# Optimization experiments

Hardware: AMD Instinct MI355X
Metric: run time of the kernel (lower is better)

Reference implementation:

```python
import jax, jax.numpy as jnp
import numpy as np

N = 50000      # nodes
E = 800000     # edges
IN = 64        # in_dim
HID = 32       # num_hidden (per head)
H1, H2, H3 = 4, 4, 6   # heads
C = 64         # num_classes
SLOPE = 0.2    # leaky relu negative slope


def setup_inputs() -> dict:
    key = jax.random.key(0)
    ks = jax.random.split(key, 13)
    p = lambda k, s: jax.random.normal(k, s, jnp.float32) * 0.05
    return {
        "src": jax.random.randint(ks[0], (E,), 0, N),
        "dst": jax.random.randint(ks[1], (E,), 0, N),
        "embed": p(ks[2], (N, IN)),
        "W0": p(ks[3], (IN, H1 * HID)),
        "al0": p(ks[4], (H1, HID)), "ar0": p(ks[5], (H1, HID)),
        "W1": p(ks[6], (H1 * HID, H2 * HID)),
        "al1": p(ks[7], (H2, HID)), "ar1": p(ks[8], (H2, HID)),
        "W2": p(ks[9], (H2 * HID, H3 * C)),
        "al2": p(ks[10], (H3, C)), "ar2": p(ks[11], (H3, C)),
        "Wres": p(ks[12], (H2 * HID, H3 * C)),
    }


def gat_conv(h, W, al, ar, src, dst, H, D, res=None):
    """One DGL-style GATConv (no dropout, eval mode)."""
    n = h.shape[0]
    feat = (h @ W).reshape(n, H, D)                      # [N,H,D]
    el = jnp.sum(feat * al, axis=-1)                     # [N,H]
    er = jnp.sum(feat * ar, axis=-1)                     # [N,H]
    e = jax.nn.leaky_relu(el[src] + er[dst], SLOPE)      # [E,H]
    # edge softmax over incoming edges of each dst node
    m = jax.lax.stop_gradient(jax.ops.segment_max(e, dst, num_segments=n))
    ex = jnp.exp(e - m[dst])
    s = jax.ops.segment_sum(ex, dst, num_segments=n)
    alpha = ex / jnp.where(s == 0.0, 1.0, s)[dst]        # [E,H]
    rst = jax.ops.segment_sum(feat[src] * alpha[:, :, None], dst, num_segments=n)
    if res is not None:
        rst = rst + res
    return rst                                           # [N,H,D]


def reference(src, dst, embed, W0, al0, ar0, W1, al1, ar1, W2, al2, ar2, Wres):
    h = embed
    # layer 0: no residual, elu, flatten heads
    h = jax.nn.elu(gat_conv(h, W0, al0, ar0, src, dst, H1, HID)).reshape(N, H1 * HID)
    # layer 1: residual is identity (in_dim == H2*HID)
    res1 = h.reshape(N, H2, HID)
    h = jax.nn.elu(gat_conv(h, W1, al1, ar1, src, dst, H2, HID, res=res1)).reshape(N, H2 * HID)
    # output layer: linear residual (dims differ), no activation, mean over heads
    res2 = (h @ Wres).reshape(N, H3, C)
    out = gat_conv(h, W2, al2, ar2, src, dst, H3, C, res=res2)
    return out.mean(axis=1)                              # [N,C]
```

## Files before the change

### kernel.cpp

```cpp
#include <hip/hip_runtime.h>
#include <hip/hip_bf16.h>
#include <cstdint>

#define NNODES 50000
#define NEDGES 800000
constexpr float SLOPE = 0.2f;

__device__ __forceinline__ float leakyf(float x){ return x > 0.f ? x : SLOPE * x; }
__device__ __forceinline__ float eluf(float x){ return x > 0.f ? x : expm1f(x); }

__global__ void hist_kernel(const int* __restrict__ dst, int* __restrict__ deg, int e){
  int i = blockIdx.x * 256 + threadIdx.x;
  if (i < e) atomicAdd(&deg[dst[i]], 1);
}

__global__ __launch_bounds__(256) void scan1_kernel(const int* __restrict__ deg,
    int* __restrict__ pre, int* __restrict__ bsum, int n){
  __shared__ int s[256];
  int t = threadIdx.x;
  int i = blockIdx.x * 256 + t;
  int v = (i < n) ? deg[i] : 0;
  s[t] = v;
  __syncthreads();
  #pragma unroll
  for (int off = 1; off < 256; off <<= 1){
    int x = (t >= off) ? s[t - off] : 0;
    __syncthreads();
    s[t] += x;
    __syncthreads();
  }
  if (i < n) pre[i] = s[t] - v;
  if (t == 255) bsum[blockIdx.x] = s[255];
}

__global__ __launch_bounds__(256) void scan2_kernel(int* __restrict__ bsum, int nb){
  __shared__ int s[256];
  int t = threadIdx.x;
  int v = (t < nb) ? bsum[t] : 0;
  s[t] = v;
  __syncthreads();
  #pragma unroll
  for (int off = 1; off < 256; off <<= 1){
    int x = (t >= off) ? s[t - off] : 0;
    __syncthreads();
    s[t] += x;
    __syncthreads();
  }
  if (t < nb) bsum[t] = s[t] - v;
}

__global__ __launch_bounds__(256) void scan3_kernel(const int* __restrict__ pre,
    const int* __restrict__ bsum, int* __restrict__ row, int* __restrict__ cur,
    int n, int etot){
  int i = blockIdx.x * 256 + threadIdx.x;
  if (i < n){
    int r = pre[i] + bsum[i >> 8];
    row[i] = r; cur[i] = r;
  }
  if (i == n) row[n] = etot;
}

__global__ void scatter_kernel(const int* __restrict__ src, const int* __restrict__ dst,
    int* __restrict__ cur, int* __restrict__ ssrc, int* __restrict__ sdst, int e){
  int i = blockIdx.x * 256 + threadIdx.x;
  if (i < e){
    int d = dst[i];
    int pos = atomicAdd(&cur[d], 1);
    ssrc[pos] = src[i];
    sdst[pos] = d;
  }
}

template<int K, bool ACC>
__global__ __launch_bounds__(256) void gemm_kernel(const float* __restrict__ A,
    const float* __restrict__ B, float* __restrict__ C, int n_rows, int n_cols){
  __shared__ float As[64][68];
  __shared__ float Bs[64][64];
  int tx = threadIdx.x & 15, ty = threadIdx.x >> 4;
  int row0 = blockIdx.x * 64, col0 = blockIdx.y * 64;
  float acc[4][4] = {};
  for (int k0 = 0; k0 < K; k0 += 64){
    for (int v = threadIdx.x; v < 1024; v += 256){
      int r = v >> 4, c = (v & 15) << 2;
      float4 val = make_float4(0.f, 0.f, 0.f, 0.f);
      int gr = row0 + r;
      if (gr < n_rows) val = *reinterpret_cast<const float4*>(&A[(size_t)gr * K + k0 + c]);
      *reinterpret_cast<float4*>(&As[r][c]) = val;
    }
    for (int v = threadIdx.x; v < 1024; v += 256){
      int r = v >> 4, c = (v & 15) << 2;
      *reinterpret_cast<float4*>(&Bs[r][c]) =
        *reinterpret_cast<const float4*>(&B[(size_t)(k0 + r) * n_cols + col0 + c]);
    }
    __syncthreads();
    #pragma unroll 8
    for (int k = 0; k < 64; ++k){
      float a[4], b[4];
      #pragma unroll
      for (int i = 0; i < 4; ++i) a[i] = As[ty * 4 + i][k];
      #pragma unroll
      for (int j = 0; j < 4; ++j) b[j] = Bs[k][tx * 4 + j];
      #pragma unroll
      for (int i = 0; i < 4; ++i)
        #pragma unroll
        for (int j = 0; j < 4; ++j)
          acc[i][j] += a[i] * b[j];
    }
    __syncthreads();
  }
  #pragma unroll
  for (int i = 0; i < 4; ++i){
    int gr = row0 + ty * 4 + i;
    if (gr < n_rows){
      float* cp = &C[(size_t)gr * n_cols + col0 + tx * 4];
      float4 v = make_float4(acc[i][0], acc[i][1], acc[i][2], acc[i][3]);
      if constexpr (ACC){
        float4 o = *reinterpret_cast<const float4*>(cp);
        v.x += o.x; v.y += o.y; v.z += o.z; v.w += o.w;
      }
      *reinterpret_cast<float4*>(cp) = v;
    }
  }
}

__global__ void wvec_kernel(const float* __restrict__ W, const float* __restrict__ al,
    const float* __restrict__ ar, float* __restrict__ wl, float* __restrict__ wr,
    int K, int H, int D){
  int idx = blockIdx.x * 256 + threadIdx.x;
  if (idx >= H * K) return;
  int h = idx / K, k = idx - h * K;
  const float* wrow = W + (size_t)k * H * D + h * D;
  const float* a = al + h * D;
  const float* b = ar + h * D;
  float sl = 0.f, sr = 0.f;
  for (int d = 0; d < D; ++d){ float wv = wrow[d]; sl += wv * a[d]; sr += wv * b[d]; }
  wl[idx] = sl; wr[idx] = sr;
}

template<int H, int K>
__global__ __launch_bounds__(256) void elrn_kernel(const float* __restrict__ x,
    const float* __restrict__ wl, const float* __restrict__ wr,
    float* __restrict__ el, float* __restrict__ er){
  __shared__ float wls[H * K], wrs[H * K];
  for (int v = threadIdx.x; v < H * K; v += 256){ wls[v] = wl[v]; wrs[v] = wr[v]; }
  __syncthreads();
  int n = blockIdx.x * 256 + threadIdx.x;
  if (n >= NNODES) return;
  const float* xr = x + (size_t)n * K;
  float accl[H] = {}, accr[H] = {};
  for (int k = 0; k < K; k += 4){
    float4 xv = *reinterpret_cast<const float4*>(xr + k);
    #pragma unroll
    for (int h = 0; h < H; ++h){
      const float* a = &wls[h * K + k];
      const float* b = &wrs[h * K + k];
      accl[h] += xv.x * a[0] + xv.y * a[1] + xv.z * a[2] + xv.w * a[3];
      accr[h] += xv.x * b[0] + xv.y * b[1] + xv.z * b[2] + xv.w * b[3];
    }
  }
  #pragma unroll
  for (int h = 0; h < H; ++h){ el[n * H + h] = accl[h]; er[n * H + h] = accr[h]; }
}

__global__ __launch_bounds__(256) void elr1_kernel(const float* __restrict__ feat,
    const float* __restrict__ al, const float* __restrict__ ar,
    float* __restrict__ el, float* __restrict__ er){
  __shared__ float als[128], ars[128];
  if (threadIdx.x < 128){ als[threadIdx.x] = al[threadIdx.x]; ars[threadIdx.x] = ar[threadIdx.x]; }
  __syncthreads();
  int n = blockIdx.x * 256 + threadIdx.x;
  if (n >= NNODES) return;
  const float* f = feat + (size_t)n * 128;
  float el4[4], er4[4];
  #pragma unroll
  for (int h = 0; h < 4; ++h){
    float sl = 0.f, sr = 0.f;
    #pragma unroll
    for (int d = 0; d < 32; d += 4){
      float4 fv = *reinterpret_cast<const float4*>(f + h * 32 + d);
      const float* a = &als[h * 32 + d];
      const float* b = &ars[h * 32 + d];
      sl += fv.x * a[0] + fv.y * a[1] + fv.z * a[2] + fv.w * a[3];
      sr += fv.x * b[0] + fv.y * b[1] + fv.z * b[2] + fv.w * b[3];
    }
    el4[h] = sl; er4[h] = sr;
  }
  *reinterpret_cast<float4*>(&el[n * 4]) = make_float4(el4[0], el4[1], el4[2], el4[3]);
  *reinterpret_cast<float4*>(&er[n * 4]) = make_float4(er4[0], er4[1], er4[2], er4[3]);
}

template<int H>
__global__ void ex_kernel(const float* __restrict__ el, const float* __restrict__ er,
    const int* __restrict__ ssrc, const int* __restrict__ sdst, float* __restrict__ ex, int e){
  int i = blockIdx.x * 256 + threadIdx.x;
  if (i >= e) return;
  int s = ssrc[i], d = sdst[i];
  if constexpr (H == 4){
    float4 a = *reinterpret_cast<const float4*>(&el[s * 4]);
    float4 b = *reinterpret_cast<const float4*>(&er[d * 4]);
    float4 o;
    o.x = expf(leakyf(a.x + b.x));
    o.y = expf(leakyf(a.y + b.y));
    o.z = expf(leakyf(a.z + b.z));
    o.w = expf(leakyf(a.w + b.w));
    *reinterpret_cast<float4*>(&ex[(size_t)i * 4]) = o;
  } else {
    const float* ap = &el[s * 6];
    const float* bp = &er[d * 6];
    float2 a0 = *reinterpret_cast<const float2*>(ap);
    float2 a1 = *reinterpret_cast<const float2*>(ap + 2);
    float2 a2 = *reinterpret_cast<const float2*>(ap + 4);
    float2 b0 = *reinterpret_cast<const float2*>(bp);
    float2 b1 = *reinterpret_cast<const float2*>(bp + 2);
    float2 b2 = *reinterpret_cast<const float2*>(bp + 4);
    float2 o0, o1, o2;
    o0.x = expf(leakyf(a0.x + b0.x)); o0.y = expf(leakyf(a0.y + b0.y));
    o1.x = expf(leakyf(a1.x + b1.x)); o1.y = expf(leakyf(a1.y + b1.y));
    o2.x = expf(leakyf(a2.x + b2.x)); o2.y = expf(leakyf(a2.y + b2.y));
    float* op = &ex[(size_t)i * 6];
    *reinterpret_cast<float2*>(op)     = o0;
    *reinterpret_cast<float2*>(op + 2) = o1;
    *reinterpret_cast<float2*>(op + 4) = o2;
  }
}

__global__ __launch_bounds__(1024) void agg_l0_kernel(const float* __restrict__ embed,
    const float* __restrict__ W0, const float* __restrict__ ex,
    const int* __restrict__ row, const int* __restrict__ ssrc, float* __restrict__ h1){
  __shared__ float W0t[128 * 68];
  __shared__ float gd[16][256];
  int w = threadIdx.x >> 6, lane = threadIdx.x & 63;
  for (int v = threadIdx.x; v < 2048; v += 1024){
    float4 val = *reinterpret_cast<const float4*>(&W0[(size_t)v << 2]);
    int k = (v << 2) >> 7;
    int c = (v << 2) & 127;
    W0t[(c + 0) * 68 + k] = val.x;
    W0t[(c + 1) * 68 + k] = val.y;
    W0t[(c + 2) * 68 + k] = val.z;
    W0t[(c + 3) * 68 + k] = val.w;
  }
  int n = blockIdx.x * 16 + w;
  int beg = __builtin_amdgcn_readfirstlane(row[n]);
  int end = __builtin_amdgcn_readfirstlane(row[n + 1]);
  float g0 = 0.f, g1 = 0.f, g2 = 0.f, g3 = 0.f;
  float t0 = 0.f, t1 = 0.f, t2 = 0.f, t3 = 0.f;
  int i = beg;
  for (; i + 8 <= end; i += 8){
    float v[8]; float4 e[8];
    #pragma unroll
    for (int u = 0; u < 8; ++u){
      int s = ssrc[i + u];
      v[u] = embed[(size_t)s * 64 + lane];
      e[u] = *reinterpret_cast<const float4*>(&ex[(size_t)(i + u) * 4]);
    }
    #pragma unroll
    for (int u = 0; u < 8; ++u){
      g0 += e[u].x * v[u]; g1 += e[u].y * v[u];
      g2 += e[u].z * v[u]; g3 += e[u].w * v[u];
      t0 += e[u].x; t1 += e[u].y; t2 += e[u].z; t3 += e[u].w;
    }
  }
  for (; i + 4 <= end; i += 4){
    float v[4]; float4 e[4];
    #pragma unroll
    for (int u = 0; u < 4; ++u){
      int s = ssrc[i + u];
      v[u] = embed[(size_t)s * 64 + lane];
      e[u] = *reinterpret_cast<const float4*>(&ex[(size_t)(i + u) * 4]);
    }
    #pragma unroll
    for (int u = 0; u < 4; ++u){
      g0 += e[u].x * v[u]; g1 += e[u].y * v[u];
      g2 += e[u].z * v[u]; g3 += e[u].w * v[u];
      t0 += e[u].x; t1 += e[u].y; t2 += e[u].z; t3 += e[u].w;
    }
  }
  for (; i < end; ++i){
    int s = ssrc[i];
    float ev = embed[(size_t)s * 64 + lane];
    float4 e = *reinterpret_cast<const float4*>(&ex[(size_t)i * 4]);
    g0 += e.x * ev; g1 += e.y * ev; g2 += e.z * ev; g3 += e.w * ev;
    t0 += e.x; t1 += e.y; t2 += e.z; t3 += e.w;
  }
  float i0 = t0 > 0.f ? 1.f / t0 : 0.f, i1 = t1 > 0.f ? 1.f / t1 : 0.f;
  float i2 = t2 > 0.f ? 1.f / t2 : 0.f, i3 = t3 > 0.f ? 1.f / t3 : 0.f;
  gd[w][lane] = g0 * i0; gd[w][64 + lane] = g1 * i1;
  gd[w][128 + lane] = g2 * i2; gd[w][192 + lane] = g3 * i3;
  __syncthreads();
  int c = threadIdx.x & 127, q = threadIdx.x >> 7;
  int h = c >> 5;
  const float4* wrow = reinterpret_cast<const float4*>(&W0t[c * 68]);
  const float4* gA = reinterpret_cast<const float4*>(&gd[2 * q][h * 64]);
  const float4* gB = reinterpret_cast<const float4*>(&gd[2 * q + 1][h * 64]);
  float o0 = 0.f, o1 = 0.f;
  #pragma unroll
  for (int k4 = 0; k4 < 16; ++k4){
    float4 wv = wrow[k4];
    float4 a = gA[k4], b = gB[k4];
    o0 += a.x * wv.x + a.y * wv.y + a.z * wv.z + a.w * wv.w;
    o1 += b.x * wv.x + b.y * wv.y + b.z * wv.z + b.w * wv.w;
  }
  int nb = blockIdx.x * 16;
  h1[(size_t)(nb + 2 * q) * 128 + c]     = eluf(o0);
  h1[(size_t)(nb + 2 * q + 1) * 128 + c] = eluf(o1);
}

__global__ __launch_bounds__(256) void agg32_kernel(const float* __restrict__ feat,
    const float* __restrict__ ex, const int* __restrict__ row, const int* __restrict__ ssrc,
    const float* __restrict__ resid, float* __restrict__ hout){
  int n = blockIdx.x * 4 + (threadIdx.x >> 6);
  if (n >= NNODES) return;
  int lane = threadIdx.x & 63, half = lane >> 5;
  int beg = __builtin_amdgcn_readfirstlane(row[n]);
  int end = __builtin_amdgcn_readfirstlane(row[n + 1]);
  float acc0 = 0.f, acc1 = 0.f, tA = 0.f, tB = 0.f;
  int i = beg;
  for (; i + 8 <= end; i += 8){
    float a[8], b[8], eA[8], eB[8];
    #pragma unroll
    for (int u = 0; u < 8; ++u){
      int s = ssrc[i + u];
      const float* fr = feat + (size_t)s * 128;
      a[u] = fr[lane]; b[u] = fr[64 + lane];
      float4 e = *reinterpret_cast<const float4*>(&ex[(size_t)(i + u) * 4]);
      eA[u] = half ? e.y : e.x;
      eB[u] = half ? e.w : e.z;
    }
    #pragma unroll
    for (int u = 0; u < 8; ++u){
      acc0 += eA[u] * a[u]; acc1 += eB[u] * b[u];
      tA += eA[u]; tB += eB[u];
    }
  }
  for (; i + 4 <= end; i += 4){
    float a[4], b[4], eA[4], eB[4];
    #pragma unroll
    for (int u = 0; u < 4; ++u){
      int s = ssrc[i + u];
      const float* fr = feat + (size_t)s * 128;
      a[u] = fr[lane]; b[u] = fr[64 + lane];
      float4 e = *reinterpret_cast<const float4*>(&ex[(size_t)(i + u) * 4]);
      eA[u] = half ? e.y : e.x;
      eB[u] = half ? e.w : e.z;
    }
    #pragma unroll
    for (int u = 0; u < 4; ++u){
      acc0 += eA[u] * a[u]; acc1 += eB[u] * b[u];
      tA += eA[u]; tB += eB[u];
    }
  }
  for (; i < end; ++i){
    int s = ssrc[i];
    const float* fr = feat + (size_t)s * 128;
    float4 e = *reinterpret_cast<const float4*>(&ex[(size_t)i * 4]);
    float eA = half ? e.y : e.x;
    float eB = half ? e.w : e.z;
    acc0 += eA * fr[lane]; acc1 += eB * fr[64 + lane];
    tA += eA; tB += eB;
  }
  float invA = tA > 0.f ? 1.f / tA : 0.f;
  float invB = tB > 0.f ? 1.f / tB : 0.f;
  float v0 = acc0 * invA, v1 = acc1 * invB;
  size_t o0 = (size_t)n * 128 + lane;
  v0 += resid[o0]; v1 += resid[o0 + 64];
  hout[o0]      = eluf(v0);
  hout[o0 + 64] = eluf(v1);
}

__global__ __launch_bounds__(256) void agg_l2_kernel(const float* __restrict__ h2,
    const float* __restrict__ ex, const int* __restrict__ row, const int* __restrict__ ssrc,
    float* __restrict__ gs, int node_off, int node_cnt){
  int rel = blockIdx.x * 4 + (threadIdx.x >> 6);
  if (rel >= node_cnt) return;
  int n = node_off + rel;
  int lane = threadIdx.x & 63;
  int beg = __builtin_amdgcn_readfirstlane(row[n]);
  int end = __builtin_amdgcn_readfirstlane(row[n + 1]);
  float t[6] = {};
  float ga[6] = {}, gb[6] = {};
  int i = beg;
  for (; i + 8 <= end; i += 8){
    float v0[8], v1[8];
    float2 ea[8], eb[8], ec[8];
    #pragma unroll
    for (int u = 0; u < 8; ++u){
      int s = ssrc[i + u];
      const float* hr = h2 + (size_t)s * 128;
      v0[u] = hr[lane]; v1[u] = hr[64 + lane];
      const float* e = &ex[(size_t)(i + u) * 6];
      ea[u] = *reinterpret_cast<const float2*>(e);
      eb[u] = *reinterpret_cast<const float2*>(e + 2);
      ec[u] = *reinterpret_cast<const float2*>(e + 4);
    }
    #pragma unroll
    for (int u = 0; u < 8; ++u){
      ga[0] += ea[u].x * v0[u]; gb[0] += ea[u].x * v1[u]; t[0] += ea[u].x;
      ga[1] += ea[u].y * v0[u]; gb[1] += ea[u].y * v1[u]; t[1] += ea[u].y;
      ga[2] += eb[u].x * v0[u]; gb[2] += eb[u].x * v1[u]; t[2] += eb[u].x;
      ga[3] += eb[u].y * v0[u]; gb[3] += eb[u].y * v1[u]; t[3] += eb[u].y;
      ga[4] += ec[u].x * v0[u]; gb[4] += ec[u].x * v1[u]; t[4] += ec[u].x;
      ga[5] += ec[u].y * v0[u]; gb[5] += ec[u].y * v1[u]; t[5] += ec[u].y;
    }
  }
  for (; i + 4 <= end; i += 4){
    float v0[4], v1[4];
    float2 ea[4], eb[4], ec[4];
    #pragma unroll
    for (int u = 0; u < 4; ++u){
      int s = ssrc[i + u];
      const float* hr = h2 + (size_t)s * 128;
      v0[u] = hr[lane]; v1[u] = hr[64 + lane];
      const float* e = &ex[(size_t)(i + u) * 6];
      ea[u] = *reinterpret_cast<const float2*>(e);
      eb[u] = *reinterpret_cast<const float2*>(e + 2);
      ec[u] = *reinterpret_cast<const float2*>(e + 4);
    }
    #pragma unroll
    for (int u = 0; u < 4; ++u){
      ga[0] += ea[u].x * v0[u]; gb[0] += ea[u].x * v1[u]; t[0] += ea[u].x;
      ga[1] += ea[u].y * v0[u]; gb[1] += ea[u].y * v1[u]; t[1] += ea[u].y;
      ga[2] += eb[u].x * v0[u]; gb[2] += eb[u].x * v1[u]; t[2] += eb[u].x;
      ga[3] += eb[u].y * v0[u]; gb[3] += eb[u].y * v1[u]; t[3] += eb[u].y;
      ga[4] += ec[u].x * v0[u]; gb[4] += ec[u].x * v1[u]; t[4] += ec[u].x;
      ga[5] += ec[u].y * v0[u]; gb[5] += ec[u].y * v1[u]; t[5] += ec[u].y;
    }
  }
  for (; i < end; ++i){
    int s = ssrc[i];
    const float* hr = h2 + (size_t)s * 128;
    float v0 = hr[lane], v1 = hr[64 + lane];
    const float* e = &ex[(size_t)i * 6];
    float2 a = *reinterpret_cast<const float2*>(e);
    float2 b = *reinterpret_cast<const float2*>(e + 2);
    float2 c = *reinterpret_cast<const float2*>(e + 4);
    ga[0] += a.x * v0; gb[0] += a.x * v1; t[0] += a.x;
    ga[1] += a.y * v0; gb[1] += a.y * v1; t[1] += a.y;
    ga[2] += b.x * v0; gb[2] += b.x * v1; t[2] += b.x;
    ga[3] += b.y * v0; gb[3] += b.y * v1; t[3] += b.y;
    ga[4] += c.x * v0; gb[4] += c.x * v1; t[4] += c.x;
    ga[5] += c.y * v0; gb[5] += c.y * v1; t[5] += c.y;
  }
  float inv[6];
  #pragma unroll
  for (int h = 0; h < 6; ++h) inv[h] = t[h] > 0.f ? 1.f / (6.f * t[h]) : 0.f;
  float* gr = gs + (size_t)rel * 768;
  #pragma unroll
  for (int h = 0; h < 6; ++h){
    gr[h * 128 + lane]      = ga[h] * inv[h];
    gr[h * 128 + 64 + lane] = gb[h] * inv[h];
  }
}

__global__ void w2r_kernel(const float* __restrict__ W2, float* __restrict__ W2r){
  int i = blockIdx.x * 256 + threadIdx.x;
  if (i >= 768 * 64) return;
  int hk = i >> 6, c = i & 63;
  int h = hk >> 7, k = hk & 127;
  W2r[i] = W2[(size_t)k * 384 + h * 64 + c];
}

__global__ void wresmean_kernel(const float* __restrict__ Wres, float* __restrict__ wm){
  int i = blockIdx.x * 256 + threadIdx.x;
  if (i < 128 * 64){
    int k = i >> 6, c = i & 63;
    float s = 0.f;
    #pragma unroll
    for (int h = 0; h < 6; ++h) s += Wres[k * 384 + h * 64 + c];
    wm[i] = s * (1.f / 6.f);
  }
}

extern "C" void kernel_launch(void* const* d_in, const int* in_sizes, int n_in,
                              void* d_out, int out_size, void* d_ws, size_t ws_size,
                              hipStream_t stream){
  const int*   src   = (const int*)d_in[0];
  const int*   dst   = (const int*)d_in[1];
  const float* embed = (const float*)d_in[2];
  const float* W0    = (const float*)d_in[3];
  const float* al0   = (const float*)d_in[4];
  const float* ar0   = (const float*)d_in[5];
  const float* W1    = (const float*)d_in[6];
  const float* al1   = (const float*)d_in[7];
  const float* ar1   = (const float*)d_in[8];
  const float* W2    = (const float*)d_in[9];
  const float* al2   = (const float*)d_in[10];
  const float* ar2   = (const float*)d_in[11];
  const float* Wres  = (const float*)d_in[12];
  float* out = (float*)d_out;

  char* p = (char*)d_ws;
  auto alloc = [&](size_t bytes) -> char* {
    char* r = p; p += (bytes + 255) & ~size_t(255); return r;
  };
  float* big  = (float*)alloc((size_t)25000 * 768 * 4);
  float* h1   = (float*)alloc((size_t)NNODES * 128 * 4);
  float* h2   = (float*)alloc((size_t)NNODES * 128 * 4);
  float* el   = (float*)alloc((size_t)NNODES * 6 * 4);
  float* er   = (float*)alloc((size_t)NNODES * 6 * 4);
  float* ex   = (float*)alloc((size_t)NEDGES * 6 * 4);
  float* wm   = (float*)alloc(128 * 64 * 4);
  float* W2r  = (float*)alloc(768 * 64 * 4);
  float* wl0  = (float*)alloc(4 * 64 * 4);
  float* wr0  = (float*)alloc(4 * 64 * 4);
  float* wl2  = (float*)alloc(6 * 128 * 4);
  float* wr2  = (float*)alloc(6 * 128 * 4);
  int* row    = (int*)alloc((NNODES + 1) * 4);
  int* cur    = (int*)alloc(NNODES * 4);
  int* deg    = (int*)alloc(NNODES * 4);
  int* pre    = (int*)alloc(NNODES * 4);
  int* bsum   = (int*)alloc(256 * 4);
  int* ssrc   = (int*)alloc(NEDGES * 4);
  int* sdst   = (int*)alloc(NEDGES * 4);

  const int NB = (NNODES + 255) / 256;

  hipMemsetAsync(deg, 0, NNODES * 4, stream);
  hist_kernel<<<(NEDGES + 255) / 256, 256, 0, stream>>>(dst, deg, NEDGES);
  scan1_kernel<<<NB, 256, 0, stream>>>(deg, pre, bsum, NNODES);
  scan2_kernel<<<1, 256, 0, stream>>>(bsum, NB);
  scan3_kernel<<<NB + 1, 256, 0, stream>>>(pre, bsum, row, cur, NNODES, NEDGES);
  scatter_kernel<<<(NEDGES + 255) / 256, 256, 0, stream>>>(src, dst, cur, ssrc, sdst, NEDGES);

  wvec_kernel<<<1, 256, 0, stream>>>(W0, al0, ar0, wl0, wr0, 64, 4, 32);
  wvec_kernel<<<3, 256, 0, stream>>>(W2, al2, ar2, wl2, wr2, 128, 6, 64);
  w2r_kernel<<<192, 256, 0, stream>>>(W2, W2r);
  wresmean_kernel<<<32, 256, 0, stream>>>(Wres, wm);

  const int GX = (NNODES + 63) / 64;
  const int GE = (NEDGES + 255) / 256;
  const int GN = (NNODES + 3) / 4;
  const int GNn = (NNODES + 255) / 256;

  elrn_kernel<4, 64><<<GNn, 256, 0, stream>>>(embed, wl0, wr0, el, er);
  ex_kernel<4><<<GE, 256, 0, stream>>>(el, er, ssrc, sdst, ex, NEDGES);
  agg_l0_kernel<<<NNODES / 16, 1024, 0, stream>>>(embed, W0, ex, row, ssrc, h1);

  gemm_kernel<128, false><<<dim3(GX, 2), 256, 0, stream>>>(h1, W1, big, NNODES, 128);
  elr1_kernel<<<GNn, 256, 0, stream>>>(big, al1, ar1, el, er);
  ex_kernel<4><<<GE, 256, 0, stream>>>(el, er, ssrc, sdst, ex, NEDGES);
  agg32_kernel<<<GN, 256, 0, stream>>>(big, ex, row, ssrc, h1, h2);

  elrn_kernel<6, 128><<<GNn, 256, 0, stream>>>(h2, wl2, wr2, el, er);
  ex_kernel<6><<<GE, 256, 0, stream>>>(el, er, ssrc, sdst, ex, NEDGES);
  gemm_kernel<128, false><<<dim3(GX, 1), 256, 0, stream>>>(h2, wm, out, NNODES, 64);
  const int HALF = 25000;
  for (int half = 0; half < 2; ++half){
    int off = half * HALF;
    agg_l2_kernel<<<(HALF + 3) / 4, 256, 0, stream>>>(h2, ex, row, ssrc, big, off, HALF);
    gemm_kernel<768, true><<<dim3((HALF + 63) / 64, 1), 256, 0, stream>>>(
        big, W2r, out + (size_t)off * 64, HALF, 64);
  }
}
```

Measured before the change: 587.8 us.

## Fill sorted dst from CSR rows and restructure layer-0 aggregation

The scatter kernel no longer writes sdst at scattered positions. A new per-node kernel fills sdst contiguously from the CSR row offsets instead. In agg_l0, the softmax denominators are computed first with a lane-parallel pass and a wave shuffle reduction, which removes the per-edge t accumulations from the main loop, and the 4-edge unrolled tail loop is dropped. W0 is now kept in shared memory in its original layout, without the transpose, and the projection loop reads it as scalars. This adds an extra kernel launch and a second read of ex per node in exchange for cheaper scatter writes and a leaner inner loop.

```diff
diff --git a/kernel.cpp b/kernel.cpp
--- a/kernel.cpp
+++ b/kernel.cpp
@@ -60,14 +60,21 @@
   if (i == n) row[n] = etot;
 }
 
+__global__ __launch_bounds__(256) void sdstfill_kernel(const int* __restrict__ row,
+    int* __restrict__ sdst){
+  int n = blockIdx.x * 4 + (threadIdx.x >> 6);
+  if (n >= NNODES) return;
+  int lane = threadIdx.x & 63;
+  int beg = row[n], end = row[n + 1];
+  for (int i = beg + lane; i < end; i += 64) sdst[i] = n;
+}
+
 __global__ void scatter_kernel(const int* __restrict__ src, const int* __restrict__ dst,
-    int* __restrict__ cur, int* __restrict__ ssrc, int* __restrict__ sdst, int e){
+    int* __restrict__ cur, int* __restrict__ ssrc, int e){
   int i = blockIdx.x * 256 + threadIdx.x;
   if (i < e){
-    int d = dst[i];
-    int pos = atomicAdd(&cur[d], 1);
+    int pos = atomicAdd(&cur[dst[i]], 1);
     ssrc[pos] = src[i];
-    sdst[pos] = d;
   }
 }
 
@@ -227,23 +234,27 @@
 __global__ __launch_bounds__(1024) void agg_l0_kernel(const float* __restrict__ embed,
     const float* __restrict__ W0, const float* __restrict__ ex,
     const int* __restrict__ row, const int* __restrict__ ssrc, float* __restrict__ h1){
-  __shared__ float W0t[128 * 68];
+  __shared__ float W0s[64 * 128];
   __shared__ float gd[16][256];
   int w = threadIdx.x >> 6, lane = threadIdx.x & 63;
-  for (int v = threadIdx.x; v < 2048; v += 1024){
-    float4 val = *reinterpret_cast<const float4*>(&W0[(size_t)v << 2]);
-    int k = (v << 2) >> 7;
-    int c = (v << 2) & 127;
-    W0t[(c + 0) * 68 + k] = val.x;
-    W0t[(c + 1) * 68 + k] = val.y;
-    W0t[(c + 2) * 68 + k] = val.z;
-    W0t[(c + 3) * 68 + k] = val.w;
-  }
+  for (int v = threadIdx.x; v < 2048; v += 1024)
+    *reinterpret_cast<float4*>(&W0s[v << 2]) = *reinterpret_cast<const float4*>(&W0[(size_t)v << 2]);
   int n = blockIdx.x * 16 + w;
   int beg = __builtin_amdgcn_readfirstlane(row[n]);
   int end = __builtin_amdgcn_readfirstlane(row[n + 1]);
+  float t0 = 0.f, t1 = 0.f, t2 = 0.f, t3 = 0.f;
+  for (int i = beg + lane; i < end; i += 64){
+    float4 e = *reinterpret_cast<const float4*>(&ex[(size_t)i * 4]);
+    t0 += e.x; t1 += e.y; t2 += e.z; t3 += e.w;
+  }
+  #pragma unroll
+  for (int o = 32; o; o >>= 1){
+    t0 += __shfl_xor(t0, o, 64); t1 += __shfl_xor(t1, o, 64);
+    t2 += __shfl_xor(t2, o, 64); t3 += __shfl_xor(t3, o, 64);
+  }
+  float i0 = t0 > 0.f ? 1.f / t0 : 0.f, i1 = t1 > 0.f ? 1.f / t1 : 0.f;
+  float i2 = t2 > 0.f ? 1.f / t2 : 0.f, i3 = t3 > 0.f ? 1.f / t3 : 0.f;
   float g0 = 0.f, g1 = 0.f, g2 = 0.f, g3 = 0.f;
-  float t0 = 0.f, t1 = 0.f, t2 = 0.f, t3 = 0.f;
   int i = beg;
   for (; i + 8 <= end; i += 8){
     float v[8]; float4 e[8];
@@ -257,22 +268,6 @@
     for (int u = 0; u < 8; ++u){
       g0 += e[u].x * v[u]; g1 += e[u].y * v[u];
       g2 += e[u].z * v[u]; g3 += e[u].w * v[u];
-      t0 += e[u].x; t1 += e[u].y; t2 += e[u].z; t3 += e[u].w;
-    }
-  }
-  for (; i + 4 <= end; i += 4){
-    float v[4]; float4 e[4];
-    #pragma unroll
-    for (int u = 0; u < 4; ++u){
-      int s = ssrc[i + u];
-      v[u] = embed[(size_t)s * 64 + lane];
-      e[u] = *reinterpret_cast<const float4*>(&ex[(size_t)(i + u) * 4]);
-    }
-    #pragma unroll
-    for (int u = 0; u < 4; ++u){
-      g0 += e[u].x * v[u]; g1 += e[u].y * v[u];
-      g2 += e[u].z * v[u]; g3 += e[u].w * v[u];
-      t0 += e[u].x; t1 += e[u].y; t2 += e[u].z; t3 += e[u].w;
     }
   }
   for (; i < end; ++i){
@@ -280,25 +275,20 @@
     float ev = embed[(size_t)s * 64 + lane];
     float4 e = *reinterpret_cast<const float4*>(&ex[(size_t)i * 4]);
     g0 += e.x * ev; g1 += e.y * ev; g2 += e.z * ev; g3 += e.w * ev;
-    t0 += e.x; t1 += e.y; t2 += e.z; t3 += e.w;
-  }
-  float i0 = t0 > 0.f ? 1.f / t0 : 0.f, i1 = t1 > 0.f ? 1.f / t1 : 0.f;
-  float i2 = t2 > 0.f ? 1.f / t2 : 0.f, i3 = t3 > 0.f ? 1.f / t3 : 0.f;
+  }
   gd[w][lane] = g0 * i0; gd[w][64 + lane] = g1 * i1;
   gd[w][128 + lane] = g2 * i2; gd[w][192 + lane] = g3 * i3;
   __syncthreads();
   int c = threadIdx.x & 127, q = threadIdx.x >> 7;
   int h = c >> 5;
-  const float4* wrow = reinterpret_cast<const float4*>(&W0t[c * 68]);
-  const float4* gA = reinterpret_cast<const float4*>(&gd[2 * q][h * 64]);
-  const float4* gB = reinterpret_cast<const float4*>(&gd[2 * q + 1][h * 64]);
+  const float* gp0 = &gd[2 * q][h * 64];
+  const float* gp1 = &gd[2 * q + 1][h * 64];
   float o0 = 0.f, o1 = 0.f;
-  #pragma unroll
-  for (int k4 = 0; k4 < 16; ++k4){
-    float4 wv = wrow[k4];
-    float4 a = gA[k4], b = gB[k4];
-    o0 += a.x * wv.x + a.y * wv.y + a.z * wv.z + a.w * wv.w;
-    o1 += b.x * wv.x + b.y * wv.y + b.z * wv.z + b.w * wv.w;
+  #pragma unroll 8
+  for (int k = 0; k < 64; ++k){
+    float wv = W0s[(k << 7) + c];
+    o0 += gp0[k] * wv;
+    o1 += gp1[k] * wv;
   }
   int nb = blockIdx.x * 16;
   h1[(size_t)(nb + 2 * q) * 128 + c]     = eluf(o0);
@@ -519,7 +509,8 @@
   scan1_kernel<<<NB, 256, 0, stream>>>(deg, pre, bsum, NNODES);
   scan2_kernel<<<1, 256, 0, stream>>>(bsum, NB);
   scan3_kernel<<<NB + 1, 256, 0, stream>>>(pre, bsum, row, cur, NNODES, NEDGES);
-  scatter_kernel<<<(NEDGES + 255) / 256, 256, 0, stream>>>(src, dst, cur, ssrc, sdst, NEDGES);
+  sdstfill_kernel<<<(NNODES + 3) / 4, 256, 0, stream>>>(row, sdst);
+  scatter_kernel<<<(NEDGES + 255) / 256, 256, 0, stream>>>(src, dst, cur, ssrc, NEDGES);
 
   wvec_kernel<<<1, 256, 0, stream>>>(W0, al0, ar0, wl0, wr0, 64, 4, 32);
   wvec_kernel<<<3, 256, 0, stream>>>(W2, al2, ar2, wl2, wr2, 128, 6, 64);
```

New measurement: 568.0 us. 1.03x faster.
